# Optimization experiments

Hardware: AMD Instinct MI355X
Metric: run time of the kernel (lower is better)

Reference implementation:

```python
import jax, jax.numpy as jnp
import numpy as np

HID, INP, BATCH, TIME = 1024, 512, 128, 256


def _kaiming(key, d1, d2, gain):
    # kaiming_normal_: std = gain / sqrt(fan_in), fan_in = d2
    return jax.random.normal(key, (d1, d2), jnp.float32) * (gain / np.sqrt(d2))


def setup_inputs() -> dict:
    key = jax.random.key(0)
    ks = jax.random.split(key, 9)
    g_lin = 1.0          # nonlinearity='linear'
    g_tanh = 5.0 / 3.0   # nonlinearity='tanh'
    inp = {
        "x": jax.random.normal(ks[0], (BATCH, TIME, INP), jnp.float32),
        "c": jnp.zeros((HID, BATCH), jnp.float32),
        "h": jnp.zeros((HID, BATCH), jnp.float32),
        "W_gx": _kaiming(ks[1], HID, INP, g_lin),
        "W_ix": _kaiming(ks[2], HID, INP, g_lin),
        "W_fx": _kaiming(ks[3], HID, INP, g_lin),
        "W_ox": _kaiming(ks[4], HID, INP, g_lin),
        "W_gh": _kaiming(ks[5], HID, HID, g_tanh),
        "W_ih": _kaiming(ks[6], HID, HID, g_tanh),
        "W_fh": _kaiming(ks[7], HID, HID, g_tanh),
        "W_oh": _kaiming(ks[8], HID, HID, g_tanh),
        "b_g": jnp.zeros((HID, 1), jnp.float32),
        "b_i": jnp.zeros((HID, 1), jnp.float32),
        "b_f": jnp.zeros((HID, 1), jnp.float32),
        "b_o": jnp.zeros((HID, 1), jnp.float32),
    }
    return inp


def reference(x, c, h, W_gx, W_ix, W_fx, W_ox, W_gh, W_ih, W_fh, W_oh,
              b_g, b_i, b_f, b_o):
    Hd = W_gx.shape[0]
    # Fuse the four gate GEMMs into one: same math, single contraction.
    Wx = jnp.concatenate([W_gx, W_ix, W_fx, W_ox], axis=0)   # (4H, I)
    Wh = jnp.concatenate([W_gh, W_ih, W_fh, W_oh], axis=0)   # (4H, H)
    b = jnp.concatenate([b_g, b_i, b_f, b_o], axis=0)[:, 0]  # (4H,)
    # Precompute all input projections: (T, B, 4H)
    xs = jnp.einsum('bti,gi->tbg', x, Wx)

    def step(carry, xt):
        c_t, h_t = carry                      # (B, H)
        z = xt + h_t @ Wh.T + b               # (B, 4H)
        g = jnp.tanh(z[:, :Hd])
        i = jax.nn.sigmoid(z[:, Hd:2 * Hd])
        f = jax.nn.sigmoid(z[:, 2 * Hd:3 * Hd])
        o = jax.nn.sigmoid(z[:, 3 * Hd:])
        c_n = g * i + c_t * f
        h_n = jnp.tanh(c_n) * o
        return (c_n, h_n), None

    (c_f, h_f), _ = jax.lax.scan(step, (c.T, h.T), xs)
    return h_f.T  # (H, B), matching the torch layout
```

## Files before the change

kernel.cpp:

```cpp
#include <hip/hip_runtime.h>
#include <cstdint>
#include <cstddef>

#define HID 1024
#define INP 512
#define BATCH 128
#define TSTEPS 256
#define NK16 96
#define HSLOTS 32
#define NBLK_CHUNK 256
#define HSLOT ((size_t)64 * 4 * 2 * 512)

using short8  = __attribute__((ext_vector_type(8))) short;
using f32x16  = __attribute__((ext_vector_type(16))) float;

#define LD8(p) (*(const short8*)(p))
#define MFMA32(a,b,c) __builtin_amdgcn_mfma_f32_32x32x16_bf16((a),(b),(c),0,0,0)

static __device__ __forceinline__ unsigned short f2bf(float f) {
    union { float f; unsigned int u; } v; v.f = f;
    unsigned int r = v.u + 0x7fffu + ((v.u >> 16) & 1u);
    return (unsigned short)(r >> 16);
}
static __device__ __forceinline__ float bf2f(unsigned short b) {
    union { unsigned int u; float f; } v; v.u = ((unsigned int)b) << 16;
    return v.f;
}
static __device__ __forceinline__ float sigmoid_f(float z) {
    return 1.0f / (1.0f + __expf(-z));
}
static __device__ __forceinline__ float tanh_f(float z) {
    return 2.0f / (1.0f + __expf(-2.0f * z)) - 1.0f;
}


__global__ void prep_w(const float* __restrict__ Wgx, const float* __restrict__ Wix,
                       const float* __restrict__ Wfx, const float* __restrict__ Wox,
                       const float* __restrict__ Wgh, const float* __restrict__ Wih,
                       const float* __restrict__ Wfh, const float* __restrict__ Woh,
                       unsigned short* __restrict__ wfrag)
{
    const int k16 = blockIdx.x;
    const int s   = blockIdx.y;
    const int tid  = threadIdx.x;
    const int lane = tid >> 2;
    const int e0   = (tid & 3) * 2;
    const int row  = s * 32 + (lane & 31);
    const int k    = k16 * 16 + (lane >> 5) * 8 + e0;
    const int j = row >> 2;
    const int g = row & 3;
    float f0, f1;
    if (k < INP) {
        const float* wx = (g == 0 ? Wgx : g == 1 ? Wix : g == 2 ? Wfx : Wox) + (size_t)j * INP;
        f0 = wx[k]; f1 = wx[k + 1];
    } else {
        const float* wh = (g == 0 ? Wgh : g == 1 ? Wih : g == 2 ? Wfh : Woh) + (size_t)j * HID;
        f0 = wh[k - INP]; f1 = wh[k - INP + 1];
    }
    ushort2 hi, lo;
    hi.x = f2bf(f0); lo.x = f2bf(f0 - bf2f(hi.x));
    hi.y = f2bf(f1); lo.y = f2bf(f1 - bf2f(hi.y));
    unsigned short* base = wfrag + ((size_t)(s * NK16 + k16) * 2) * 512 + lane * 8 + e0;
    *(ushort2*)(base)       = hi;
    *(ushort2*)(base + 512) = lo;
}

__global__ void prep_x(const float* __restrict__ x, unsigned short* __restrict__ xfrag)
{
    const int k16x = blockIdx.x;
    const int t    = blockIdx.y;
    const int tid  = threadIdx.x;
    const int cg   = tid >> 6;
    const int lane = tid & 63;
    const int col  = cg * 32 + (lane & 31);
    const int k0   = k16x * 16 + (lane >> 5) * 8;
    const float* src = x + ((size_t)col * TSTEPS + t) * INP + k0;
    const float4 v0 = *(const float4*)(src);
    const float4 v1 = *(const float4*)(src + 4);
    ushort4 h0, l0, h1, l1;
    h0.x = f2bf(v0.x); l0.x = f2bf(v0.x - bf2f(h0.x));
    h0.y = f2bf(v0.y); l0.y = f2bf(v0.y - bf2f(h0.y));
    h0.z = f2bf(v0.z); l0.z = f2bf(v0.z - bf2f(h0.z));
    h0.w = f2bf(v0.w); l0.w = f2bf(v0.w - bf2f(h0.w));
    h1.x = f2bf(v1.x); l1.x = f2bf(v1.x - bf2f(h1.x));
    h1.y = f2bf(v1.y); l1.y = f2bf(v1.y - bf2f(h1.y));
    h1.z = f2bf(v1.z); l1.z = f2bf(v1.z - bf2f(h1.z));
    h1.w = f2bf(v1.w); l1.w = f2bf(v1.w - bf2f(h1.w));
    unsigned short* base = xfrag +
        ((size_t)(((size_t)t * 32 + k16x) * 4 + cg) * 2) * 512 + lane * 8;
    *(ushort4*)(base)           = h0;
    *(ushort4*)(base + 4)       = h1;
    *(ushort4*)(base + 512)     = l0;
    *(ushort4*)(base + 512 + 4) = l1;
}

__global__ void prep_state(const float* __restrict__ cin, const float* __restrict__ hin,
                           float* __restrict__ cdst, unsigned short* __restrict__ hslot,
                           unsigned* __restrict__ flags)
{
    if (blockIdx.x == 0) flags[threadIdx.x] = 0u;
    const int idx = blockIdx.x * 256 + threadIdx.x;
    cdst[idx] = cin[idx];
    const int j = idx >> 7;
    const int b = idx & 127;
    float f = hin[idx];
    unsigned short hh = f2bf(f);
    unsigned short hl = f2bf(f - bf2f(hh));
    const int k16h = j >> 4;
    const int hlf  = (j >> 3) & 1;
    const int e    = j & 7;
    const int cg   = b >> 5;
    const int lane = 32 * hlf + (b & 31);
    unsigned short* base = hslot +
        ((size_t)((k16h * 4 + cg) * 2) * 512) + lane * 8 + e;
    base[0]   = hh;
    base[512] = hl;
}

__global__ __launch_bounds__(512, 1) void lstm_persist(
    const unsigned short* __restrict__ wfrag,
    const unsigned short* __restrict__ xfrag,
    unsigned short* __restrict__ hbuf,
    float* __restrict__ cst,
    const float* __restrict__ bg, const float* __restrict__ bi,
    const float* __restrict__ bf_, const float* __restrict__ bo,
    float* __restrict__ outf,
    unsigned* __restrict__ flags)
{
    const int tid  = threadIdx.x;
    const int wv   = tid >> 6;
    const int lane = tid & 63;
    const int l31  = lane & 31;
    const int hl   = lane >> 5;
    const int bx   = blockIdx.x;

    const int xcd     = bx & 7;
    const int ii      = bx >> 3;
    const int s       = xcd * 16 + (ii >> 1);
    const int cb      = ii & 1;
    const int colbase = cb << 6;

    const int ejl  = tid >> 6;
    const int ecl  = tid & 63;
    const int ej   = s * 8 + ejl;
    const int ecol = colbase + ecl;
    const size_t ci = (size_t)ej * BATCH + ecol;

    const float bias0 = bg[ej], bias1 = bi[ej], bias2 = bf_[ej], bias3 = bo[ej];
    float creg = cst[ci];

    const size_t bOff = (size_t)(4 * wv + 2 * cb) * 1024 + lane * 8;
    const int k16h = s >> 1;

    __shared__ unsigned short WhLds[65536];
    __shared__ float part[3][32][64];
    __shared__ unsigned long long hstage[256];
    unsigned short* hs16 = (unsigned short*)hstage;

    {
        const unsigned short* src = wfrag + (size_t)(s * NK16 + 32) * 2 * 512;
#pragma unroll
        for (int c = 0; c < 16; ++c) {
            const int cid = c * 512 + tid;
            *(short8*)(WhLds + (size_t)cid * 8) = LD8(src + (size_t)cid * 8);
        }
    }
    short8 wxh[4], wxl[4];
    {
        const unsigned short* pWx = wfrag + ((size_t)(s * NK16 + wv) * 2) * 512 + lane * 8;
#pragma unroll
        for (int m = 0; m < 4; ++m) {
            wxh[m] = LD8(pWx);
            wxl[m] = LD8(pWx + 512);
            pWx += 8192;
        }
    }
    short8 xb0h[4], xb0l[4], xb1h[4], xb1l[4];
    {
        const unsigned short* pX = xfrag + bOff;
#pragma unroll
        for (int m = 0; m < 4; ++m) {
            xb0h[m] = LD8(pX);
            xb0l[m] = LD8(pX + 512);
            xb1h[m] = LD8(pX + 1024);
            xb1l[m] = LD8(pX + 1536);
            pX += 32768;
        }
    }
    __syncthreads();

#pragma unroll 1
    for (int t = 0; t < TSTEPS; ++t) {
        if (t > 0) {
            const unsigned target = (unsigned)t;
            int done;
            int guard = 0;
            do {
                unsigned v = target;
                if (tid < 256)
                    v = __hip_atomic_load(&flags[tid], __ATOMIC_RELAXED,
                                          __HIP_MEMORY_SCOPE_AGENT);
                done = __syncthreads_count(v >= target);
                if (done < 512) __builtin_amdgcn_s_sleep(1);
            } while (done < 512 && ++guard < (1 << 20));
            asm volatile("" ::: "memory");
            __builtin_amdgcn_sched_barrier(0);
            if ((t & 31) == 0)
                __builtin_amdgcn_fence(__ATOMIC_ACQUIRE, "agent");
        }

        f32x16 a0A, a0B, a1A, a1B;
#pragma unroll
        for (int r = 0; r < 16; ++r) { a0A[r]=0.f; a0B[r]=0.f; a1A[r]=0.f; a1B[r]=0.f; }

        const unsigned short* pH = hbuf
            + (size_t)((t + HSLOTS - 1) & (HSLOTS - 1)) * HSLOT + bOff;

        short8 hb0h[8], hb0l[8], hb1h[8], hb1l[8];
#pragma unroll
        for (int m = 0; m < 4; ++m) {
            hb0h[m] = LD8(pH);
            hb0l[m] = LD8(pH + 512);
            hb1h[m] = LD8(pH + 1024);
            hb1l[m] = LD8(pH + 1536);
            pH += 32768;
        }

#pragma unroll
        for (int m = 0; m < 4; ++m) {
            a0A = MFMA32(wxh[m], xb0h[m], a0A);
            a1A = MFMA32(wxh[m], xb1h[m], a1A);
            a0B = MFMA32(wxh[m], xb0l[m], a0B);
            a1B = MFMA32(wxh[m], xb1l[m], a1B);
            a0A = MFMA32(wxl[m], xb0h[m], a0A);
            a1A = MFMA32(wxl[m], xb1h[m], a1A);
        }

#pragma unroll
        for (int m = 4; m < 8; ++m) {
            hb0h[m] = LD8(pH);
            hb0l[m] = LD8(pH + 512);
            hb1h[m] = LD8(pH + 1024);
            hb1l[m] = LD8(pH + 1536);
            pH += 32768;
        }

#pragma unroll
        for (int m = 0; m < 8; ++m) {
            const unsigned short* wp = WhLds + (size_t)((8 * m + wv) * 2) * 512 + lane * 8;
            short8 Ah = *(const short8*)(wp);
            short8 Al = *(const short8*)(wp + 512);
            a0A = MFMA32(Ah, hb0h[m], a0A);
            a1A = MFMA32(Ah, hb1h[m], a1A);
            a0B = MFMA32(Ah, hb0l[m], a0B);
            a1B = MFMA32(Ah, hb1l[m], a1B);
            a0A = MFMA32(Al, hb0h[m], a0A);
            a1A = MFMA32(Al, hb1h[m], a1A);
        }

        if (wv >= 5) {
#pragma unroll
            for (int r = 0; r < 16; ++r) {
                const int lr = (r & 3) + 8 * (r >> 2) + 4 * hl;
                part[wv - 5][lr][l31]      = a0A[r] + a0B[r];
                part[wv - 5][lr][32 + l31] = a1A[r] + a1B[r];
            }
        }
        __syncthreads();
        if (wv >= 2 && wv < 5) {
#pragma unroll
            for (int r = 0; r < 16; ++r) {
                const int lr = (r & 3) + 8 * (r >> 2) + 4 * hl;
                part[wv - 2][lr][l31]      += a0A[r] + a0B[r];
                part[wv - 2][lr][32 + l31] += a1A[r] + a1B[r];
            }
        }
        __syncthreads();
        if (wv < 2) {
#pragma unroll
            for (int r = 0; r < 16; ++r) {
                const int lr = (r & 3) + 8 * (r >> 2) + 4 * hl;
                part[wv][lr][l31]      += a0A[r] + a0B[r];
                part[wv][lr][32 + l31] += a1A[r] + a1B[r];
            }
        }
        __syncthreads();

        {
            const int r0 = 4 * ejl;
            float z0g = bias0 + part[0][r0 + 0][ecl] + part[1][r0 + 0][ecl] + part[2][r0 + 0][ecl];
            float z1g = bias1 + part[0][r0 + 1][ecl] + part[1][r0 + 1][ecl] + part[2][r0 + 1][ecl];
            float z2g = bias2 + part[0][r0 + 2][ecl] + part[1][r0 + 2][ecl] + part[2][r0 + 2][ecl];
            float z3g = bias3 + part[0][r0 + 3][ecl] + part[1][r0 + 3][ecl] + part[2][r0 + 3][ecl];
            float gg = tanh_f(z0g);
            float ig = sigmoid_f(z1g);
            float fg = sigmoid_f(z2g);
            float og = sigmoid_f(z3g);
            float cn = gg * ig + creg * fg;
            creg = cn;
            float hh = tanh_f(cn) * og;
            unsigned short hb  = f2bf(hh);
            unsigned short hlo = f2bf(hh - bf2f(hb));
            hs16[((ecl >> 5) * 2 + 0) * 256 + (ecl & 31) * 8 + ejl] = hb;
            hs16[((ecl >> 5) * 2 + 1) * 256 + (ecl & 31) * 8 + ejl] = hlo;
            if (outf && t == TSTEPS - 1) outf[ci] = hh;
        }
        __syncthreads();

        {
            unsigned short* hout = hbuf + (size_t)(t & (HSLOTS - 1)) * HSLOT;
            if (tid < 256) {
                const int r   = tid >> 6;
                const int w   = tid & 63;
                const int cgg = 2 * cb + (r >> 1);
                const int p   = r & 1;
                const size_t uo = ((size_t)((k16h * 4 + cgg) * 2 + p)) * 512
                                + 32 * (s & 1) * 8 + w * 4;
                __hip_atomic_store((unsigned long long*)(hout + uo), hstage[tid],
                                   __ATOMIC_RELAXED, __HIP_MEMORY_SCOPE_AGENT);
            }
        }
        asm volatile("s_waitcnt vmcnt(0)" ::: "memory");
        __syncthreads();
        if (tid == 0)
            __hip_atomic_store(&flags[bx], (unsigned)(t + 1),
                               __ATOMIC_RELAXED, __HIP_MEMORY_SCOPE_AGENT);

        {
            const int tn = (t + 1 < TSTEPS) ? (t + 1) : t;
            const unsigned short* pX = xfrag + (size_t)tn * 131072 + bOff;
#pragma unroll
            for (int m = 0; m < 4; ++m) {
                xb0h[m] = LD8(pX);
                xb0l[m] = LD8(pX + 512);
                xb1h[m] = LD8(pX + 1024);
                xb1l[m] = LD8(pX + 1536);
                pX += 32768;
            }
        }
    }
    cst[ci] = creg;
}

__global__ __launch_bounds__(512, 1) void lstm_step(
    const unsigned short* __restrict__ wfrag,
    const unsigned short* __restrict__ xfrag,
    const unsigned short* __restrict__ hin,
    unsigned short* __restrict__ hout,
    float* __restrict__ cst,
    const float* __restrict__ bg, const float* __restrict__ bi,
    const float* __restrict__ bf_, const float* __restrict__ bo,
    float* __restrict__ outf, int t)
{
    const int tid  = threadIdx.x;
    const int wv   = tid >> 6;
    const int lane = tid & 63;
    const int l31  = lane & 31;
    const int hl   = lane >> 5;
    const int bx   = blockIdx.x;

    const int xcd     = bx & 7;
    const int ii      = bx >> 3;
    const int s       = xcd * 16 + (ii >> 1);
    const int cb      = ii & 1;
    const int colbase = cb << 6;

    const int ejl  = tid >> 6;
    const int ecl  = tid & 63;
    const int ej   = s * 8 + ejl;
    const int ecol = colbase + ecl;

    float add0 = bg[ej], add1 = bi[ej], add2 = bf_[ej], add3 = bo[ej];
    const size_t ci = (size_t)ej * BATCH + ecol;
    float cold = cst[ci];

    f32x16 a0A, a0B, a1A, a1B;
#pragma unroll
    for (int r = 0; r < 16; ++r) { a0A[r]=0.f; a0B[r]=0.f; a1A[r]=0.f; a1B[r]=0.f; }

    const size_t bOff = (size_t)(4 * wv + 2 * cb) * 1024 + lane * 8;

    {
        const unsigned short* pA = wfrag + ((size_t)(s * NK16 + wv) * 2) * 512 + lane * 8;
        const unsigned short* pX = xfrag + (size_t)t * 131072 + bOff;
#pragma unroll
        for (int m = 0; m < 4; ++m) {
            short8 Ah  = LD8(pA);
            short8 Al  = LD8(pA + 512);
            short8 B0h = LD8(pX);
            short8 B0l = LD8(pX + 512);
            short8 B1h = LD8(pX + 1024);
            short8 B1l = LD8(pX + 1536);
            pA += 8192; pX += 32768;
            a0A = MFMA32(Ah, B0h, a0A);
            a1A = MFMA32(Ah, B1h, a1A);
            a0B = MFMA32(Ah, B0l, a0B);
            a1B = MFMA32(Ah, B1l, a1B);
            a0A = MFMA32(Al, B0h, a0A);
            a1A = MFMA32(Al, B1h, a1A);
        }
        const unsigned short* pH = hin + bOff;
#pragma unroll
        for (int m = 0; m < 8; ++m) {
            short8 Ah  = LD8(pA);
            short8 Al  = LD8(pA + 512);
            short8 B0h = LD8(pH);
            short8 B0l = LD8(pH + 512);
            short8 B1h = LD8(pH + 1024);
            short8 B1l = LD8(pH + 1536);
            pA += 8192; pH += 32768;
            a0A = MFMA32(Ah, B0h, a0A);
            a1A = MFMA32(Ah, B1h, a1A);
            a0B = MFMA32(Ah, B0l, a0B);
            a1B = MFMA32(Ah, B1l, a1B);
            a0A = MFMA32(Al, B0h, a0A);
            a1A = MFMA32(Al, B1h, a1A);
        }
    }

    __shared__ float part[8][32][64];
#pragma unroll
    for (int r = 0; r < 16; ++r) {
        const int lr = (r & 3) + 8 * (r >> 2) + 4 * hl;
        part[wv][lr][l31]      = a0A[r] + a0B[r];
        part[wv][lr][32 + l31] = a1A[r] + a1B[r];
    }
    __syncthreads();

    {
        const int r0 = 4 * ejl;
        float z0g = add0, z1g = add1, z2g = add2, z3g = add3;
#pragma unroll
        for (int p = 0; p < 8; ++p) {
            z0g += part[p][r0 + 0][ecl];
            z1g += part[p][r0 + 1][ecl];
            z2g += part[p][r0 + 2][ecl];
            z3g += part[p][r0 + 3][ecl];
        }
        float gg = tanh_f(z0g);
        float ig = sigmoid_f(z1g);
        float fg = sigmoid_f(z2g);
        float og = sigmoid_f(z3g);
        float cn = gg * ig + cold * fg;
        cst[ci] = cn;
        float hh = tanh_f(cn) * og;
        unsigned short hb  = f2bf(hh);
        unsigned short hlo = f2bf(hh - bf2f(hb));
        const int k16h  = s >> 1;
        const int cgg   = (colbase >> 5) + (ecl >> 5);
        const int lane8 = 32 * (s & 1) + (ecl & 31);
        unsigned short* dst = hout +
            ((size_t)((k16h * 4 + cgg) * 2) * 512) + lane8 * 8 + ejl;
        dst[0]   = hb;
        dst[512] = hlo;
        if (outf) outf[ci] = hh;
    }
}

extern "C" void kernel_launch(void* const* d_in, const int* in_sizes, int n_in,
                              void* d_out, int out_size, void* d_ws, size_t ws_size,
                              hipStream_t stream)
{
    const float* x   = (const float*)d_in[0];
    const float* c0v = (const float*)d_in[1];
    const float* h0v = (const float*)d_in[2];
    const float* Wgx = (const float*)d_in[3];
    const float* Wix = (const float*)d_in[4];
    const float* Wfx = (const float*)d_in[5];
    const float* Wox = (const float*)d_in[6];
    const float* Wgh = (const float*)d_in[7];
    const float* Wih = (const float*)d_in[8];
    const float* Wfh = (const float*)d_in[9];
    const float* Woh = (const float*)d_in[10];
    const float* bg  = (const float*)d_in[11];
    const float* bi  = (const float*)d_in[12];
    const float* bf  = (const float*)d_in[13];
    const float* bo  = (const float*)d_in[14];

    unsigned short* wfrag = (unsigned short*)d_ws;
    unsigned short* xfrag = wfrag + (size_t)128 * NK16 * 2 * 512;
    unsigned short* hbuf  = xfrag + (size_t)TSTEPS * 32 * 4 * 2 * 512;
    float* cst            = (float*)(hbuf + (size_t)HSLOTS * HSLOT);
    unsigned* flags       = (unsigned*)(cst + (size_t)HID * BATCH);

    const size_t needA = (size_t)((char*)(flags + 1024) - (char*)d_ws);
    const bool useA = (ws_size >= needA);

    float* outp = (float*)d_out;

    prep_w<<<dim3(NK16, 128), dim3(256), 0, stream>>>(Wgx, Wix, Wfx, Wox,
                                                      Wgh, Wih, Wfh, Woh, wfrag);
    prep_x<<<dim3(32, TSTEPS), dim3(256), 0, stream>>>(x, xfrag);
    prep_state<<<dim3(512), dim3(256), 0, stream>>>(c0v, h0v, cst,
                                                    hbuf + (size_t)(HSLOTS - 1) * HSLOT,
                                                    flags);

    bool done = false;
    if (useA) {
        const unsigned short* a_wfrag = wfrag;
        const unsigned short* a_xfrag = xfrag;
        unsigned short* a_hbuf = hbuf;
        float* a_cst = cst;
        const float* a_bg = bg; const float* a_bi = bi;
        const float* a_bf = bf; const float* a_bo = bo;
        float* a_out = outp;
        unsigned* a_flags = flags;
        void* kargs[] = { (void*)&a_wfrag, (void*)&a_xfrag, (void*)&a_hbuf,
                          (void*)&a_cst, (void*)&a_bg, (void*)&a_bi,
                          (void*)&a_bf, (void*)&a_bo, (void*)&a_out,
                          (void*)&a_flags };
        hipError_t ce = hipLaunchCooperativeKernel(
            (const void*)lstm_persist, dim3(NBLK_CHUNK), dim3(512),
            kargs, 0, stream);
        done = (ce == hipSuccess);
    }

    if (!done) {
        unsigned short* hfA = hbuf + (size_t)(HSLOTS - 1) * HSLOT;
        unsigned short* hfB = hbuf + (size_t)(HSLOTS - 2) * HSLOT;
        for (int t = 0; t < TSTEPS; ++t) {
            const unsigned short* hin = (t & 1) ? hfB : hfA;
            unsigned short* hout      = (t & 1) ? hfA : hfB;
            lstm_step<<<dim3(256), dim3(512), 0, stream>>>(
                wfrag, xfrag, hin, hout,
                cst, bg, bi, bf, bo,
                (t == TSTEPS - 1) ? outp : nullptr, t);
        }
    }
}
```

Before: 2.160 ms.

## Replace block-wide flag polling with per-wave targeted dependency waits

Each wavefront now polls only the producer flags for the h fragments it actually reads, computed via a per-lane index, and spins with a wave ballot instead of a block-wide __syncthreads_count over all 256 flags. The x-projection MFMAs are issued before the wait so input work overlaps with waiting on other blocks. The x loads move from a prefetch at the end of the previous step to the start of the current step. This is meant to cut the cost of the grid-wide barrier and to let waves proceed independently, at the risk of exposing x-load latency and getting the dependency mapping wrong.

New measurement: 2.873 ms. 33.0% more time.

```diff
diff --git a/kernel.cpp b/kernel.cpp
--- a/kernel.cpp
+++ b/kernel.cpp
@@ -152,6 +152,15 @@
     const size_t bOff = (size_t)(4 * wv + 2 * cb) * 1024 + lane * 8;
     const int k16h = s >> 1;
 
+    int fidx;
+    {
+        const int i5 = lane & 15;
+        const int mm = i5 >> 1;
+        const int jj = i5 & 1;
+        const int sp = 2 * (8 * mm + wv) + jj;
+        fidx = ((sp & 15) * 2 + cb) * 8 + (sp >> 4);
+    }
+
     __shared__ unsigned short WhLds[65536];
     __shared__ float part[3][32][64];
     __shared__ unsigned long long hstage[256];
@@ -175,87 +184,88 @@
             pWx += 8192;
         }
     }
-    short8 xb0h[4], xb0l[4], xb1h[4], xb1l[4];
-    {
-        const unsigned short* pX = xfrag + bOff;
-#pragma unroll
-        for (int m = 0; m < 4; ++m) {
-            xb0h[m] = LD8(pX);
-            xb0l[m] = LD8(pX + 512);
-            xb1h[m] = LD8(pX + 1024);
-            xb1l[m] = LD8(pX + 1536);
-            pX += 32768;
-        }
-    }
     __syncthreads();
 
 #pragma unroll 1
     for (int t = 0; t < TSTEPS; ++t) {
+        const unsigned target = (unsigned)t;
+        unsigned fv = 0;
+        if (t > 0)
+            fv = __hip_atomic_load(&flags[fidx], __ATOMIC_RELAXED,
+                                   __HIP_MEMORY_SCOPE_AGENT);
+
+        f32x16 a0A, a0B, a1A, a1B;
+#pragma unroll
+        for (int r = 0; r < 16; ++r) { a0A[r]=0.f; a0B[r]=0.f; a1A[r]=0.f; a1B[r]=0.f; }
+
+        {
+            const unsigned short* pX = xfrag + (size_t)t * 131072 + bOff;
+            short8 xh0[4], xl0[4], xh1[4], xl1[4];
+#pragma unroll
+            for (int m = 0; m < 4; ++m) {
+                xh0[m] = LD8(pX);
+                xl0[m] = LD8(pX + 512);
+                xh1[m] = LD8(pX + 1024);
+                xl1[m] = LD8(pX + 1536);
+                pX += 32768;
+            }
+#pragma unroll
+            for (int m = 0; m < 4; ++m) {
+                a0A = MFMA32(wxh[m], xh0[m], a0A);
+                a1A = MFMA32(wxh[m], xh1[m], a1A);
+                a0B = MFMA32(wxh[m], xl0[m], a0B);
+                a1B = MFMA32(wxh[m], xl1[m], a1B);
+                a0A = MFMA32(wxl[m], xh0[m], a0A);
+                a1A = MFMA32(wxl[m], xh1[m], a1A);
+            }
+        }
+
         if (t > 0) {
-            const unsigned target = (unsigned)t;
-            int done;
             int guard = 0;
-            do {
-                unsigned v = target;
-                if (tid < 256)
-                    v = __hip_atomic_load(&flags[tid], __ATOMIC_RELAXED,
-                                          __HIP_MEMORY_SCOPE_AGENT);
-                done = __syncthreads_count(v >= target);
-                if (done < 512) __builtin_amdgcn_s_sleep(1);
-            } while (done < 512 && ++guard < (1 << 20));
+            while (__ballot(fv >= target) != ~0ull) {
+                if (++guard > (1 << 20)) break;
+                __builtin_amdgcn_s_sleep(1);
+                fv = __hip_atomic_load(&flags[fidx], __ATOMIC_RELAXED,
+                                       __HIP_MEMORY_SCOPE_AGENT);
+            }
             asm volatile("" ::: "memory");
             __builtin_amdgcn_sched_barrier(0);
             if ((t & 31) == 0)
                 __builtin_amdgcn_fence(__ATOMIC_ACQUIRE, "agent");
         }
 
-        f32x16 a0A, a0B, a1A, a1B;
-#pragma unroll
-        for (int r = 0; r < 16; ++r) { a0A[r]=0.f; a0B[r]=0.f; a1A[r]=0.f; a1B[r]=0.f; }
-
-        const unsigned short* pH = hbuf
-            + (size_t)((t + HSLOTS - 1) & (HSLOTS - 1)) * HSLOT + bOff;
-
-        short8 hb0h[8], hb0l[8], hb1h[8], hb1l[8];
-#pragma unroll
-        for (int m = 0; m < 4; ++m) {
-            hb0h[m] = LD8(pH);
-            hb0l[m] = LD8(pH + 512);
-            hb1h[m] = LD8(pH + 1024);
-            hb1l[m] = LD8(pH + 1536);
-            pH += 32768;
-        }
-
-#pragma unroll
-        for (int m = 0; m < 4; ++m) {
-            a0A = MFMA32(wxh[m], xb0h[m], a0A);
-            a1A = MFMA32(wxh[m], xb1h[m], a1A);
-            a0B = MFMA32(wxh[m], xb0l[m], a0B);
-            a1B = MFMA32(wxh[m], xb1l[m], a1B);
-            a0A = MFMA32(wxl[m], xb0h[m], a0A);
-            a1A = MFMA32(wxl[m], xb1h[m], a1A);
-        }
-
-#pragma unroll
-        for (int m = 4; m < 8; ++m) {
-            hb0h[m] = LD8(pH);
-            hb0l[m] = LD8(pH + 512);
-            hb1h[m] = LD8(pH + 1024);
-            hb1l[m] = LD8(pH + 1536);
-            pH += 32768;
-        }
-
-#pragma unroll
-        for (int m = 0; m < 8; ++m) {
-            const unsigned short* wp = WhLds + (size_t)((8 * m + wv) * 2) * 512 + lane * 8;
-            short8 Ah = *(const short8*)(wp);
-            short8 Al = *(const short8*)(wp + 512);
-            a0A = MFMA32(Ah, hb0h[m], a0A);
-            a1A = MFMA32(Ah, hb1h[m], a1A);
-            a0B = MFMA32(Ah, hb0l[m], a0B);
-            a1B = MFMA32(Ah, hb1l[m], a1B);
-            a0A = MFMA32(Al, hb0h[m], a0A);
-            a1A = MFMA32(Al, hb1h[m], a1A);
+        {
+            const unsigned short* pH = hbuf
+                + (size_t)((t + HSLOTS - 1) & (HSLOTS - 1)) * HSLOT + bOff;
+            short8 hb0h[8], hb0l[8], hb1h[8], hb1l[8];
+#pragma unroll
+            for (int m = 0; m < 4; ++m) {
+                hb0h[m] = LD8(pH);
+                hb0l[m] = LD8(pH + 512);
+                hb1h[m] = LD8(pH + 1024);
+                hb1l[m] = LD8(pH + 1536);
+                pH += 32768;
+            }
+#pragma unroll
+            for (int m = 4; m < 8; ++m) {
+                hb0h[m] = LD8(pH);
+                hb0l[m] = LD8(pH + 512);
+                hb1h[m] = LD8(pH + 1024);
+                hb1l[m] = LD8(pH + 1536);
+                pH += 32768;
+            }
+#pragma unroll
+            for (int m = 0; m < 8; ++m) {
+                const unsigned short* wp = WhLds + (size_t)((8 * m + wv) * 2) * 512 + lane * 8;
+                short8 Ah = *(const short8*)(wp);
+                short8 Al = *(const short8*)(wp + 512);
+                a0A = MFMA32(Ah, hb0h[m], a0A);
+                a1A = MFMA32(Ah, hb1h[m], a1A);
+                a0B = MFMA32(Ah, hb0l[m], a0B);
+                a1B = MFMA32(Ah, hb1l[m], a1B);
+                a0A = MFMA32(Al, hb0h[m], a0A);
+                a1A = MFMA32(Al, hb1h[m], a1A);
+            }
         }
 
         if (wv >= 5) {
@@ -325,19 +335,6 @@
         if (tid == 0)
             __hip_atomic_store(&flags[bx], (unsigned)(t + 1),
                                __ATOMIC_RELAXED, __HIP_MEMORY_SCOPE_AGENT);
-
-        {
-            const int tn = (t + 1 < TSTEPS) ? (t + 1) : t;
-            const unsigned short* pX = xfrag + (size_t)tn * 131072 + bOff;
-#pragma unroll
-            for (int m = 0; m < 4; ++m) {
-                xb0h[m] = LD8(pX);
-                xb0l[m] = LD8(pX + 512);
-                xb1h[m] = LD8(pX + 1024);
-                xb1l[m] = LD8(pX + 1536);
-                pX += 32768;
-            }
-        }
     }
     cst[ci] = creg;
 }
```
